# Performance work log

Hardware: AMD Instinct MI355X
Metric: run time of the kernel (lower is better)

Reference implementation:

```python
import jax, jax.numpy as jnp
import numpy as np

N, E, F_IN, HID, HEADS, NCLS = 50000, 800000, 512, 64, 4, 40
NEG_SLOPE = 0.2


def setup_inputs() -> dict:
    key = jax.random.key(0)
    ks = jax.random.split(key, 12)
    x = jax.random.normal(ks[0], (N, F_IN), jnp.float32)
    edge_index = jax.random.randint(ks[1], (2, E), 0, N, jnp.int32)
    edge_weight = jnp.ones((E,), jnp.float32)
    s1 = 1.0 / np.sqrt(F_IN)
    s2 = 1.0 / np.sqrt(HID * HEADS)
    return {
        "x": x,
        "edge_index": edge_index,
        "edge_weight": edge_weight,
        "W1": jax.random.normal(ks[2], (F_IN, HEADS * HID), jnp.float32) * s1,
        "a_src1": jax.random.normal(ks[3], (HEADS, HID), jnp.float32) * s1,
        "a_dst1": jax.random.normal(ks[4], (HEADS, HID), jnp.float32) * s1,
        "b1": jnp.zeros((HEADS * HID,), jnp.float32),
        "W2": jax.random.normal(ks[5], (HEADS * HID, NCLS), jnp.float32) * s2,
        "a_src2": jax.random.normal(ks[6], (1, NCLS), jnp.float32) * s2,
        "a_dst2": jax.random.normal(ks[7], (1, NCLS), jnp.float32) * s2,
        "b2": jnp.zeros((NCLS,), jnp.float32),
    }


def _gat_layer(x, src, dst, ew, W, a_s, a_d, b, heads, n):
    c = W.shape[1] // heads
    h = (x @ W).reshape(n, heads, c)                      # [N,H,C]
    alpha_s = jnp.einsum('nhc,hc->nh', h, a_s)            # [N,H]
    alpha_d = jnp.einsum('nhc,hc->nh', h, a_d)
    e = jax.nn.leaky_relu(alpha_s[src] + alpha_d[dst], NEG_SLOPE)  # [Et,H]
    # segment softmax over destination nodes (self-loops guarantee nonempty segs)
    m = jax.ops.segment_max(e, dst, num_segments=n)
    ex = jnp.exp(e - m[dst])
    denom = jax.ops.segment_sum(ex, dst, num_segments=n)
    alpha = ex / (denom[dst] + 1e-16)                     # [Et,H]
    alpha = alpha * ew[:, None]
    msg = h[src] * alpha[:, :, None]                      # [Et,H,C]
    out = jax.ops.segment_sum(msg, dst, num_segments=n)   # [N,H,C]
    return out.reshape(n, heads * c) + b


def reference(x, edge_index, edge_weight, W1, a_src1, a_dst1, b1, W2, a_src2, a_dst2, b2):
    n = x.shape[0]
    loop = jnp.arange(n, dtype=edge_index.dtype)
    src = jnp.concatenate([edge_index[0], loop])
    dst = jnp.concatenate([edge_index[1], loop])
    ew = jnp.concatenate([edge_weight, jnp.ones((n,), edge_weight.dtype)])
    h = _gat_layer(x, src, dst, ew, W1, a_src1, a_dst1, b1, HEADS, n)
    h = jax.nn.relu(h)  # dropout p=0.0, eval mode: no-op
    out = _gat_layer(h, src, dst, ew, W2, a_src2, a_dst2, b2, 1, n)
    return out  # Identity (log_softmax_return=False)
```

## Files before the change

kernel.cpp:

```cpp
#include <hip/hip_runtime.h>
#include <math.h>

#define N_NODES 50000
#define N_EDGES 800000
#define ET (N_EDGES + N_NODES)
#define F_IN 512
#define HID 64
#define HEADS 4
#define C1 (HEADS * HID)
#define NCLS 40
#define NEG_SLOPE 0.2f

#define BUK_SHIFT 9
#define BUK_NODES (1 << BUK_SHIFT)
#define NBUK ((N_NODES + BUK_NODES - 1) / BUK_NODES)
#define CAP 16384
#define NREP 4
#define SUBCAP (CAP / NREP)
#define BF_STRIDE 8
#define EPB_A 2048
#define NBLK_A ((ET + EPB_A - 1) / EPB_A)

typedef __attribute__((ext_vector_type(8))) short short8;
typedef __attribute__((ext_vector_type(4))) float floatx4;

__device__ __forceinline__ float leaky(float x) { return fmaxf(x, NEG_SLOPE * x); }

__device__ __forceinline__ unsigned short f2bf(float f) {
    unsigned u = __float_as_uint(f);
    u += 0x7fffu + ((u >> 16) & 1u);
    return (unsigned short)(u >> 16);
}
__device__ __forceinline__ float bf2f(unsigned short u) {
    return __uint_as_float(((unsigned)u) << 16);
}
__device__ __forceinline__ float bflo(unsigned v) { return __uint_as_float(v << 16); }
__device__ __forceinline__ float bfhi(unsigned v) { return __uint_as_float(v & 0xffff0000u); }

__device__ __forceinline__ void edge_sd(int e, const int* __restrict__ ei,
                                        const float* __restrict__ ew,
                                        int& s, int& d, float& w) {
    if (e < N_EDGES) { s = ei[e]; d = ei[N_EDGES + e]; w = ew[e]; }
    else             { s = d = e - N_EDGES; w = 1.f; }
}

__global__ __launch_bounds__(256) void passA_kernel(const int* __restrict__ ei,
                                                    const float* __restrict__ ew,
                                                    int* __restrict__ cnt,
                                                    int* __restrict__ bfill,
                                                    int2* __restrict__ SB) {
    __shared__ int lcnt[NBUK];
    __shared__ int lbase[NBUK];
    const int t = threadIdx.x;
    const int rep = blockIdx.x & (NREP - 1);
    const int e0 = blockIdx.x * EPB_A + t;
    for (int i = t; i < NBUK; i += 256) lcnt[i] = 0;
    __syncthreads();
    int rx[8], ry[8];
    #pragma unroll
    for (int i = 0; i < 8; i++) {
        int e = e0 + i * 256;
        rx[i] = -1;
        ry[i] = 0;
        if (e < ET) {
            int s, d; float w;
            edge_sd(e, ei, ew, s, d, w);
            rx[i] = s | (d << 16);
            ry[i] = __float_as_int(w);
            atomicAdd(&cnt[d], 1);
            atomicAdd(&lcnt[d >> BUK_SHIFT], 1);
        }
    }
    __syncthreads();
    for (int i = t; i < NBUK; i += 256) {
        int c = lcnt[i];
        lbase[i] = c ? atomicAdd(&bfill[(i * NREP + rep) * BF_STRIDE], c) : 0;
        lcnt[i] = 0;
    }
    __syncthreads();
    #pragma unroll
    for (int i = 0; i < 8; i++) {
        if (rx[i] != -1) {
            int b = ((unsigned)rx[i] >> 16) >> BUK_SHIFT;
            int r = atomicAdd(&lcnt[b], 1);
            int idx = lbase[b] + r;
            if (idx < SUBCAP)
                SB[(size_t)b * CAP + rep * SUBCAP + idx] = make_int2(rx[i], ry[i]);
        }
    }
}

__global__ void chunk_sum_kernel(const int* __restrict__ cnt, int* __restrict__ sums) {
    __shared__ int sm[512];
    int i = blockIdx.x * 512 + threadIdx.x;
    sm[threadIdx.x] = (i < N_NODES) ? cnt[i] : 0;
    __syncthreads();
    for (int s = 256; s > 0; s >>= 1) {
        if (threadIdx.x < s) sm[threadIdx.x] += sm[threadIdx.x + s];
        __syncthreads();
    }
    if (threadIdx.x == 0) sums[blockIdx.x] = sm[0];
}

__global__ void scan_sums_kernel(int* __restrict__ sums) {
    __shared__ int sm[128];
    int i = threadIdx.x;
    int v = (i < NBUK) ? sums[i] : 0;
    sm[i] = v;
    __syncthreads();
    #pragma unroll
    for (int s = 1; s < 128; s <<= 1) {
        int t = (i >= s) ? sm[i - s] : 0;
        __syncthreads();
        sm[i] += t;
        __syncthreads();
    }
    if (i < NBUK) sums[i] = sm[i] - v;
}

__global__ __launch_bounds__(512) void rowptr_kernel(const int* __restrict__ cnt,
                                                     const int* __restrict__ sums,
                                                     int* __restrict__ row_ptr) {
    __shared__ int sm[512];
    int i = blockIdx.x * 512 + threadIdx.x;
    int v = (i < N_NODES) ? cnt[i] : 0;
    sm[threadIdx.x] = v;
    __syncthreads();
    #pragma unroll
    for (int s = 1; s < 512; s <<= 1) {
        int t = (threadIdx.x >= s) ? sm[threadIdx.x - s] : 0;
        __syncthreads();
        sm[threadIdx.x] += t;
        __syncthreads();
    }
    int excl = sm[threadIdx.x] - v + sums[blockIdx.x];
    if (i < N_NODES) row_ptr[i] = excl;
}

__global__ __launch_bounds__(1024) void place_kernel(const int* __restrict__ row_ptr,
                                                     const int* __restrict__ bfill,
                                                     const int2* __restrict__ SB,
                                                     int2* __restrict__ E2) {
    __shared__ int lfill[BUK_NODES];
    int b = blockIdx.x;
    int n0 = b << BUK_SHIFT;
    int t = threadIdx.x;
    if (t < BUK_NODES) {
        int node = n0 + t;
        lfill[t] = (node < N_NODES) ? row_ptr[node] : 0;
    }
    __syncthreads();
    for (int rep = 0; rep < NREP; rep++) {
        int c = bfill[(b * NREP + rep) * BF_STRIDE];
        if (c > SUBCAP) c = SUBCAP;
        const int2* base = SB + (size_t)b * CAP + rep * SUBCAP;
        for (int i = t; i < c; i += 1024) {
            int2 rec = base[i];
            int d = ((unsigned)rec.x) >> 16;
            int pos = atomicAdd(&lfill[d - n0], 1);
            E2[pos] = make_int2(rec.x & 0xffff, rec.y);
        }
    }
}

__global__ void wt_prep_kernel(const float* __restrict__ W, unsigned short* __restrict__ WT) {
    __shared__ float tile[32][33];
    int k0 = blockIdx.x * 32;
    int n0 = blockIdx.y * 32;
    int tx = threadIdx.x, ty = threadIdx.y;
    #pragma unroll
    for (int i = 0; i < 32; i += 8)
        tile[ty + i][tx] = W[(size_t)(k0 + ty + i) * C1 + n0 + tx];
    __syncthreads();
    #pragma unroll
    for (int i = 0; i < 32; i += 8)
        WT[(size_t)(n0 + ty + i) * F_IN + k0 + tx] = f2bf(tile[tx][ty + i]);
}

__global__ __launch_bounds__(512) void gemm1_mfma_kernel(const float* __restrict__ X,
                                                         const unsigned short* __restrict__ WT,
                                                         const float* __restrict__ a_s1,
                                                         const float* __restrict__ a_d1,
                                                         unsigned short* __restrict__ H,
                                                         float* __restrict__ AS,
                                                         float* __restrict__ AD) {
    __shared__ short As[128][40];
    __shared__ short Bs[256][40];
    const int t = threadIdx.x;
    const int m0 = blockIdx.x * 128;
    const int lane = t & 63;
    const int wave = t >> 6;
    const int wm = wave >> 2;
    const int wn = wave & 3;
    const int l15 = lane & 15;
    const int quad = lane >> 4;

    const int ar = t >> 2;
    const int ac0 = (t & 3) * 8;
    const int gr = m0 + ar;
    const int bn = t >> 1;
    const int bc0 = (t & 1) * 16;

    floatx4 acc[4][4];
    #pragma unroll
    for (int i = 0; i < 4; i++)
        #pragma unroll
        for (int j = 0; j < 4; j++) acc[i][j] = (floatx4){0.f, 0.f, 0.f, 0.f};

    for (int k0 = 0; k0 < F_IN; k0 += 32) {
        float xv[8];
        if (gr < N_NODES) {
            const float4* p = (const float4*)(X + (size_t)gr * F_IN + k0 + ac0);
            float4 v0 = p[0], v1 = p[1];
            xv[0] = v0.x; xv[1] = v0.y; xv[2] = v0.z; xv[3] = v0.w;
            xv[4] = v1.x; xv[5] = v1.y; xv[6] = v1.z; xv[7] = v1.w;
        } else {
            #pragma unroll
            for (int i = 0; i < 8; i++) xv[i] = 0.f;
        }
        short8 av;
        #pragma unroll
        for (int i = 0; i < 8; i++) av[i] = (short)f2bf(xv[i]);
        *(short8*)&As[ar][ac0] = av;

        const short8* q = (const short8*)(WT + (size_t)bn * F_IN + k0 + bc0);
        *(short8*)&Bs[bn][bc0]     = q[0];
        *(short8*)&Bs[bn][bc0 + 8] = q[1];
        __syncthreads();

        short8 a[4], b[4];
        #pragma unroll
        for (int i = 0; i < 4; i++)
            a[i] = *(const short8*)&As[wm * 64 + i * 16 + l15][quad * 8];
        #pragma unroll
        for (int j = 0; j < 4; j++)
            b[j] = *(const short8*)&Bs[wn * 64 + j * 16 + l15][quad * 8];
        #pragma unroll
        for (int i = 0; i < 4; i++)
            #pragma unroll
            for (int j = 0; j < 4; j++)
                acc[i][j] = __builtin_amdgcn_mfma_f32_16x16x32_bf16(a[i], b[j], acc[i][j], 0, 0, 0);
        __syncthreads();
    }

    float asr[4], adr[4];
    #pragma unroll
    for (int j = 0; j < 4; j++) {
        asr[j] = a_s1[wn * HID + j * 16 + l15];
        adr[j] = a_d1[wn * HID + j * 16 + l15];
    }

    #pragma unroll
    for (int i = 0; i < 4; i++) {
        int rbase = m0 + wm * 64 + i * 16 + quad * 4;
        #pragma unroll
        for (int j = 0; j < 4; j++) {
            int col = wn * 64 + j * 16 + l15;
            #pragma unroll
            for (int r = 0; r < 4; r++) {
                int row = rbase + r;
                if (row < N_NODES) H[(size_t)row * C1 + col] = f2bf(acc[i][j][r]);
            }
        }
        #pragma unroll
        for (int r = 0; r < 4; r++) {
            int row = rbase + r;
            float s_ = acc[i][0][r] * asr[0] + acc[i][1][r] * asr[1]
                     + acc[i][2][r] * asr[2] + acc[i][3][r] * asr[3];
            float d_ = acc[i][0][r] * adr[0] + acc[i][1][r] * adr[1]
                     + acc[i][2][r] * adr[2] + acc[i][3][r] * adr[3];
            #pragma unroll
            for (int m = 8; m; m >>= 1) { s_ += __shfl_xor(s_, m); d_ += __shfl_xor(d_, m); }
            if (l15 == 0 && row < N_NODES) {
                AS[row * 4 + wn] = s_;
                AD[row * 4 + wn] = d_;
            }
        }
    }
}

__global__ __launch_bounds__(256, 6) void agg1_csr_kernel(const int* __restrict__ row_ptr,
                                                          const int2* __restrict__ E2,
                                                          const float* __restrict__ AS,
                                                          const float* __restrict__ AD,
                                                          const unsigned short* __restrict__ H,
                                                          const float* __restrict__ b1,
                                                          unsigned short* __restrict__ OUT) {
    int n = blockIdx.x * 4 + (threadIdx.x >> 6);
    int lane = threadIdx.x & 63;
    if (n >= N_NODES) return;
    int l15 = lane & 15;
    int h = lane >> 4;
    int c0 = lane * 4;
    int beg = row_ptr[n];
    int end = (n + 1 < N_NODES) ? row_ptr[n + 1] : ET;
    float ad = AD[n * 4 + h];
    float den = 0.f;
    float a0 = 0.f, a1 = 0.f, a2 = 0.f, a3 = 0.f;

    for (int base = beg; base < end; base += 16) {
        int m = end - base; if (m > 16) m = 16;
        float pw = 0.f; int s = 0;
        if (l15 < m) {
            int2 e = E2[base + l15];
            s = e.x;
            float pe = __expf(leaky(AS[e.x * 4 + h] + ad));
            den += pe;
            pw = pe * __int_as_float(e.y);
        }
        int p = 0;
        for (; p + 8 <= m; p += 8) {
            int s0 = __shfl(s, p);
            int s1 = __shfl(s, p + 1);
            int s2 = __shfl(s, p + 2);
            int s3 = __shfl(s, p + 3);
            int s4 = __shfl(s, p + 4);
            int s5 = __shfl(s, p + 5);
            int s6 = __shfl(s, p + 6);
            int s7 = __shfl(s, p + 7);
            uint2 u0 = *(const uint2*)(H + (size_t)s0 * C1 + c0);
            uint2 u1 = *(const uint2*)(H + (size_t)s1 * C1 + c0);
            uint2 u2 = *(const uint2*)(H + (size_t)s2 * C1 + c0);
            uint2 u3 = *(const uint2*)(H + (size_t)s3 * C1 + c0);
            uint2 u4 = *(const uint2*)(H + (size_t)s4 * C1 + c0);
            uint2 u5 = *(const uint2*)(H + (size_t)s5 * C1 + c0);
            uint2 u6 = *(const uint2*)(H + (size_t)s6 * C1 + c0);
            uint2 u7 = *(const uint2*)(H + (size_t)s7 * C1 + c0);
            float w0 = __shfl(pw, h * 16 + p);
            float w1 = __shfl(pw, h * 16 + p + 1);
            float w2 = __shfl(pw, h * 16 + p + 2);
            float w3 = __shfl(pw, h * 16 + p + 3);
            float w4 = __shfl(pw, h * 16 + p + 4);
            float w5 = __shfl(pw, h * 16 + p + 5);
            float w6 = __shfl(pw, h * 16 + p + 6);
            float w7 = __shfl(pw, h * 16 + p + 7);
            a0 += w0 * bflo(u0.x) + w1 * bflo(u1.x) + w2 * bflo(u2.x) + w3 * bflo(u3.x)
                + w4 * bflo(u4.x) + w5 * bflo(u5.x) + w6 * bflo(u6.x) + w7 * bflo(u7.x);
            a1 += w0 * bfhi(u0.x) + w1 * bfhi(u1.x) + w2 * bfhi(u2.x) + w3 * bfhi(u3.x)
                + w4 * bfhi(u4.x) + w5 * bfhi(u5.x) + w6 * bfhi(u6.x) + w7 * bfhi(u7.x);
            a2 += w0 * bflo(u0.y) + w1 * bflo(u1.y) + w2 * bflo(u2.y) + w3 * bflo(u3.y)
                + w4 * bflo(u4.y) + w5 * bflo(u5.y) + w6 * bflo(u6.y) + w7 * bflo(u7.y);
            a3 += w0 * bfhi(u0.y) + w1 * bfhi(u1.y) + w2 * bfhi(u2.y) + w3 * bfhi(u3.y)
                + w4 * bfhi(u4.y) + w5 * bfhi(u5.y) + w6 * bfhi(u6.y) + w7 * bfhi(u7.y);
        }
        for (; p < m; p++) {
            int s0 = __shfl(s, p);
            uint2 u0 = *(const uint2*)(H + (size_t)s0 * C1 + c0);
            float w0 = __shfl(pw, h * 16 + p);
            a0 += w0 * bflo(u0.x);
            a1 += w0 * bfhi(u0.x);
            a2 += w0 * bflo(u0.y);
            a3 += w0 * bfhi(u0.y);
        }
    }
    den += __shfl_xor(den, 1);
    den += __shfl_xor(den, 2);
    den += __shfl_xor(den, 4);
    den += __shfl_xor(den, 8);

    float r = 1.f / (den + 1e-16f);
    float4 bv = *(const float4*)(b1 + c0);
    float v0 = a0 * r + bv.x, v1 = a1 * r + bv.y, v2 = a2 * r + bv.z, v3 = a3 * r + bv.w;
    v0 = v0 > 0.f ? v0 : 0.f;
    v1 = v1 > 0.f ? v1 : 0.f;
    v2 = v2 > 0.f ? v2 : 0.f;
    v3 = v3 > 0.f ? v3 : 0.f;
    uint2 o;
    o.x = ((unsigned)f2bf(v1) << 16) | (unsigned)f2bf(v0);
    o.y = ((unsigned)f2bf(v3) << 16) | (unsigned)f2bf(v2);
    *(uint2*)(OUT + (size_t)n * C1 + c0) = o;
}

#define BROW 264
__global__ __launch_bounds__(512) void gemm2_mfma_kernel(const unsigned short* __restrict__ A,
                                                         const float* __restrict__ W2,
                                                         const float* __restrict__ a_s2,
                                                         const float* __restrict__ a_d2,
                                                         unsigned short* __restrict__ H2b,
                                                         float* __restrict__ AS2,
                                                         float* __restrict__ AD2) {
    __shared__ short As[256][40];
    __shared__ short Bs[48 * BROW];
    const int t = threadIdx.x;
    const int m0 = blockIdx.x * 256;
    const int lane = t & 63;
    const int wave = t >> 6;
    const int l15 = lane & 15;
    const int quad = lane >> 4;

    for (int i = t; i < 48 * 256; i += 512) {
        int n = i >> 8, k = i & 255;
        float v = (n < NCLS) ? W2[k * NCLS + n] : 0.f;
        Bs[n * BROW + k] = (short)f2bf(v);
    }

    const int ar = t >> 1;
    const int ac0 = (t & 1) * 16;

    floatx4 acc[2][3];
    #pragma unroll
    for (int i = 0; i < 2; i++)
        #pragma unroll
        for (int j = 0; j < 3; j++) acc[i][j] = (floatx4){0.f, 0.f, 0.f, 0.f};

    for (int k0 = 0; k0 < C1; k0 += 32) {
        const short8* q = (const short8*)(A + (size_t)(m0 + ar) * C1 + k0 + ac0);
        short8 v0 = q[0], v1 = q[1];
        __syncthreads();
        *(short8*)&As[ar][ac0]     = v0;
        *(short8*)&As[ar][ac0 + 8] = v1;
        __syncthreads();

        short8 a[2], b[3];
        #pragma unroll
        for (int i = 0; i < 2; i++)
            a[i] = *(const short8*)&As[wave * 32 + i * 16 + l15][quad * 8];
        #pragma unroll
        for (int j = 0; j < 3; j++)
            b[j] = *(const short8*)&Bs[(j * 16 + l15) * BROW + k0 + quad * 8];
        #pragma unroll
        for (int i = 0; i < 2; i++)
            #pragma unroll
            for (int j = 0; j < 3; j++)
                acc[i][j] = __builtin_amdgcn_mfma_f32_16x16x32_bf16(a[i], b[j], acc[i][j], 0, 0, 0);
    }

    float asr[3], adr[3];
    #pragma unroll
    for (int j = 0; j < 3; j++) {
        int col = j * 16 + l15;
        asr[j] = (col < NCLS) ? a_s2[col] : 0.f;
        adr[j] = (col < NCLS) ? a_d2[col] : 0.f;
    }

    #pragma unroll
    for (int i = 0; i < 2; i++) {
        #pragma unroll
        for (int r = 0; r < 4; r++) {
            int row = m0 + wave * 32 + i * 16 + quad * 4 + r;
            float s_ = acc[i][0][r] * asr[0] + acc[i][1][r] * asr[1] + acc[i][2][r] * asr[2];
            float d_ = acc[i][0][r] * adr[0] + acc[i][1][r] * adr[1] + acc[i][2][r] * adr[2];
            #pragma unroll
            for (int m = 8; m; m >>= 1) { s_ += __shfl_xor(s_, m); d_ += __shfl_xor(d_, m); }
            if (l15 == 0 && row < N_NODES) { AS2[row] = s_; AD2[row] = d_; }
            #pragma unroll
            for (int j = 0; j < 3; j++) {
                int col = j * 16 + l15;
                if (col < NCLS && row < N_NODES)
                    H2b[(size_t)row * NCLS + col] = f2bf(acc[i][j][r]);
            }
        }
    }
}

__global__ __launch_bounds__(256) void agg2_csr_kernel(const int* __restrict__ row_ptr,
                                                       const int2* __restrict__ E2,
                                                       const float* __restrict__ AS,
                                                       const float* __restrict__ AD,
                                                       const unsigned short* __restrict__ H2b,
                                                       const float* __restrict__ b2,
                                                       float* __restrict__ OUT) {
    int lane = threadIdx.x & 63;
    int n = blockIdx.x * 4 + (threadIdx.x >> 6);
    if (n >= N_NODES) return;
    int beg = row_ptr[n];
    int end = (n + 1 < N_NODES) ? row_ptr[n + 1] : ET;
    float ad = AD[n];
    bool act = lane < NCLS;
    float den = 0.f, acc = 0.f;

    for (int base = beg; base < end; base += 64) {
        int m = end - base; if (m > 64) m = 64;
        float pw = 0.f; int s = 0;
        if (lane < m) {
            int2 e = E2[base + lane];
            s = e.x;
            float pe = __expf(leaky(AS[e.x] + ad));
            den += pe;
            pw = pe * __int_as_float(e.y);
        }
        int p = 0;
        for (; p + 4 <= m; p += 4) {
            int s0 = __shfl(s, p);
            int s1 = __shfl(s, p + 1);
            int s2 = __shfl(s, p + 2);
            int s3 = __shfl(s, p + 3);
            float w0 = __shfl(pw, p);
            float w1 = __shfl(pw, p + 1);
            float w2 = __shfl(pw, p + 2);
            float w3 = __shfl(pw, p + 3);
            if (act) {
                float h0 = bf2f(H2b[(size_t)s0 * NCLS + lane]);
                float h1 = bf2f(H2b[(size_t)s1 * NCLS + lane]);
                float h2 = bf2f(H2b[(size_t)s2 * NCLS + lane]);
                float h3 = bf2f(H2b[(size_t)s3 * NCLS + lane]);
                acc += w0 * h0 + w1 * h1 + w2 * h2 + w3 * h3;
            }
        }
        for (; p < m; p++) {
            int s0 = __shfl(s, p);
            float w0 = __shfl(pw, p);
            if (act) acc += w0 * bf2f(H2b[(size_t)s0 * NCLS + lane]);
        }
    }
    den += __shfl_xor(den, 1);
    den += __shfl_xor(den, 2);
    den += __shfl_xor(den, 4);
    den += __shfl_xor(den, 8);
    den += __shfl_xor(den, 16);
    den += __shfl_xor(den, 32);
    if (act) {
        float r = 1.f / (den + 1e-16f);
        OUT[(size_t)n * NCLS + lane] = acc * r + b2[lane];
    }
}

extern "C" void kernel_launch(void* const* d_in, const int* in_sizes, int n_in,
                              void* d_out, int out_size, void* d_ws, size_t ws_size,
                              hipStream_t stream) {
    const float* x    = (const float*)d_in[0];
    const int*   ei   = (const int*)d_in[1];
    const float* ew   = (const float*)d_in[2];
    const float* W1   = (const float*)d_in[3];
    const float* a_s1 = (const float*)d_in[4];
    const float* a_d1 = (const float*)d_in[5];
    const float* b1   = (const float*)d_in[6];
    const float* W2   = (const float*)d_in[7];
    const float* a_s2 = (const float*)d_in[8];
    const float* a_d2 = (const float*)d_in[9];
    const float* b2   = (const float*)d_in[10];
    float* out = (float*)d_out;

    unsigned short* H1b  = (unsigned short*)d_ws;
    unsigned short* OUT1b = H1b + (size_t)N_NODES * C1;
    float* AS1  = (float*)(OUT1b + (size_t)N_NODES * C1);
    float* AD1  = AS1 + N_NODES * HEADS;
    int* row_ptr = (int*)(AD1 + N_NODES * HEADS);
    int* cnt  = row_ptr + N_NODES;
    int* bfill = cnt + N_NODES;
    int2* E2  = (int2*)(bfill + NBUK * NREP * BF_STRIDE);
    int* sums = (int*)(E2 + ET);
    unsigned short* WT = (unsigned short*)(sums + NBUK);
    unsigned short* H2b = H1b;
    float* AS2  = (float*)(H2b + (size_t)N_NODES * NCLS);
    float* AD2  = AS2 + N_NODES;
    int2* SB = (int2*)H1b;

    hipMemsetAsync(cnt, 0, (N_NODES + NBUK * NREP * BF_STRIDE) * sizeof(int), stream);
    wt_prep_kernel<<<dim3(F_IN / 32, C1 / 32), dim3(32, 8), 0, stream>>>(W1, WT);
    passA_kernel<<<NBLK_A, 256, 0, stream>>>(ei, ew, cnt, bfill, SB);
    chunk_sum_kernel<<<NBUK, 512, 0, stream>>>(cnt, sums);
    scan_sums_kernel<<<1, 128, 0, stream>>>(sums);
    rowptr_kernel<<<NBUK, 512, 0, stream>>>(cnt, sums, row_ptr);
    place_kernel<<<NBUK, 1024, 0, stream>>>(row_ptr, bfill, SB, E2);

    gemm1_mfma_kernel<<<(N_NODES + 127) / 128, 512, 0, stream>>>(x, WT, a_s1, a_d1, H1b, AS1, AD1);
    agg1_csr_kernel<<<(N_NODES + 3) / 4, 256, 0, stream>>>(row_ptr, E2, AS1, AD1, H1b, b1, OUT1b);

    gemm2_mfma_kernel<<<(N_NODES + 255) / 256, 512, 0, stream>>>(OUT1b, W2, a_s2, a_d2, H2b, AS2, AD2);
    agg2_csr_kernel<<<(N_NODES + 3) / 4, 256, 0, stream>>>(row_ptr, E2, AS2, AD2, H2b, b2, out);
}
```

Before: 362.0 us.

## Split layer-1 aggregation into per-XCD feature halves for L2 locality

The layer-1 aggregation kernel now splits each node's 256 features into two halves handled by separate blocks. The blocks are mapped so that XCDs 0-3 process the first half (heads 0-1) and XCDs 4-7 the second half. Each XCD's L2 then only caches half of the gathered H rows, which improves its hit rate on random neighbor gathers. In exchange, edge indices and attention exponentials are recomputed in both halves, and each gather load becomes narrower (4 bytes per lane instead of 8).

```diff
diff --git a/kernel.cpp b/kernel.cpp
--- a/kernel.cpp
+++ b/kernel.cpp
@@ -279,32 +279,38 @@
     }
 }
 
-__global__ __launch_bounds__(256, 6) void agg1_csr_kernel(const int* __restrict__ row_ptr,
-                                                          const int2* __restrict__ E2,
-                                                          const float* __restrict__ AS,
-                                                          const float* __restrict__ AD,
-                                                          const unsigned short* __restrict__ H,
-                                                          const float* __restrict__ b1,
-                                                          unsigned short* __restrict__ OUT) {
-    int n = blockIdx.x * 4 + (threadIdx.x >> 6);
-    int lane = threadIdx.x & 63;
-    if (n >= N_NODES) return;
-    int l15 = lane & 15;
-    int h = lane >> 4;
-    int c0 = lane * 4;
+__global__ __launch_bounds__(256, 8) void agg1_half_kernel(const int* __restrict__ row_ptr,
+                                                           const int2* __restrict__ E2,
+                                                           const float* __restrict__ AS,
+                                                           const float* __restrict__ AD,
+                                                           const unsigned short* __restrict__ H,
+                                                           const float* __restrict__ b1,
+                                                           unsigned short* __restrict__ OUT) {
+    const int i = blockIdx.x;
+    const int xcd = i & 7;
+    const int half = xcd >> 2;
+    const int ng = (i >> 3) * 4 + (xcd & 3);
+    const int wave = threadIdx.x >> 6;
+    const int n = ng * 4 + wave;
+    const int lane = threadIdx.x & 63;
+    const int l31 = lane & 31;
+    const int hh = lane >> 5;
+    const int head = half * 2 + hh;
+    const int c0 = half * 128 + lane * 2;
+    const unsigned short* Hc = H + c0;
+
     int beg = row_ptr[n];
     int end = (n + 1 < N_NODES) ? row_ptr[n + 1] : ET;
-    float ad = AD[n * 4 + h];
-    float den = 0.f;
-    float a0 = 0.f, a1 = 0.f, a2 = 0.f, a3 = 0.f;
-
-    for (int base = beg; base < end; base += 16) {
-        int m = end - base; if (m > 16) m = 16;
+    float ad = AD[n * 4 + head];
+    float den = 0.f, a0 = 0.f, a1 = 0.f;
+
+    for (int base = beg; base < end; base += 32) {
+        int m = end - base; if (m > 32) m = 32;
         float pw = 0.f; int s = 0;
-        if (l15 < m) {
-            int2 e = E2[base + l15];
+        if (l31 < m) {
+            int2 e = E2[base + l31];
             s = e.x;
-            float pe = __expf(leaky(AS[e.x * 4 + h] + ad));
+            float pe = __expf(leaky(AS[e.x * 4 + head] + ad));
             den += pe;
             pw = pe * __int_as_float(e.y);
         }
@@ -318,57 +324,48 @@
             int s5 = __shfl(s, p + 5);
             int s6 = __shfl(s, p + 6);
             int s7 = __shfl(s, p + 7);
-            uint2 u0 = *(const uint2*)(H + (size_t)s0 * C1 + c0);
-            uint2 u1 = *(const uint2*)(H + (size_t)s1 * C1 + c0);
-            uint2 u2 = *(const uint2*)(H + (size_t)s2 * C1 + c0);
-            uint2 u3 = *(const uint2*)(H + (size_t)s3 * C1 + c0);
-            uint2 u4 = *(const uint2*)(H + (size_t)s4 * C1 + c0);
-            uint2 u5 = *(const uint2*)(H + (size_t)s5 * C1 + c0);
-            uint2 u6 = *(const uint2*)(H + (size_t)s6 * C1 + c0);
-            uint2 u7 = *(const uint2*)(H + (size_t)s7 * C1 + c0);
-            float w0 = __shfl(pw, h * 16 + p);
-            float w1 = __shfl(pw, h * 16 + p + 1);
-            float w2 = __shfl(pw, h * 16 + p + 2);
-            float w3 = __shfl(pw, h * 16 + p + 3);
-            float w4 = __shfl(pw, h * 16 + p + 4);
-            float w5 = __shfl(pw, h * 16 + p + 5);
-            float w6 = __shfl(pw, h * 16 + p + 6);
-            float w7 = __shfl(pw, h * 16 + p + 7);
-            a0 += w0 * bflo(u0.x) + w1 * bflo(u1.x) + w2 * bflo(u2.x) + w3 * bflo(u3.x)
-                + w4 * bflo(u4.x) + w5 * bflo(u5.x) + w6 * bflo(u6.x) + w7 * bflo(u7.x);
-            a1 += w0 * bfhi(u0.x) + w1 * bfhi(u1.x) + w2 * bfhi(u2.x) + w3 * bfhi(u3.x)
-                + w4 * bfhi(u4.x) + w5 * bfhi(u5.x) + w6 * bfhi(u6.x) + w7 * bfhi(u7.x);
-            a2 += w0 * bflo(u0.y) + w1 * bflo(u1.y) + w2 * bflo(u2.y) + w3 * bflo(u3.y)
-                + w4 * bflo(u4.y) + w5 * bflo(u5.y) + w6 * bflo(u6.y) + w7 * bflo(u7.y);
-            a3 += w0 * bfhi(u0.y) + w1 * bfhi(u1.y) + w2 * bfhi(u2.y) + w3 * bfhi(u3.y)
-                + w4 * bfhi(u4.y) + w5 * bfhi(u5.y) + w6 * bfhi(u6.y) + w7 * bfhi(u7.y);
+            unsigned u0 = *(const unsigned*)(Hc + (size_t)s0 * C1);
+            unsigned u1 = *(const unsigned*)(Hc + (size_t)s1 * C1);
+            unsigned u2 = *(const unsigned*)(Hc + (size_t)s2 * C1);
+            unsigned u3 = *(const unsigned*)(Hc + (size_t)s3 * C1);
+            unsigned u4 = *(const unsigned*)(Hc + (size_t)s4 * C1);
+            unsigned u5 = *(const unsigned*)(Hc + (size_t)s5 * C1);
+            unsigned u6 = *(const unsigned*)(Hc + (size_t)s6 * C1);
+            unsigned u7 = *(const unsigned*)(Hc + (size_t)s7 * C1);
+            float w0 = __shfl(pw, hh * 32 + p);
+            float w1 = __shfl(pw, hh * 32 + p + 1);
+            float w2 = __shfl(pw, hh * 32 + p + 2);
+            float w3 = __shfl(pw, hh * 32 + p + 3);
+            float w4 = __shfl(pw, hh * 32 + p + 4);
+            float w5 = __shfl(pw, hh * 32 + p + 5);
+            float w6 = __shfl(pw, hh * 32 + p + 6);
+            float w7 = __shfl(pw, hh * 32 + p + 7);
+            a0 += w0 * bflo(u0) + w1 * bflo(u1) + w2 * bflo(u2) + w3 * bflo(u3)
+                + w4 * bflo(u4) + w5 * bflo(u5) + w6 * bflo(u6) + w7 * bflo(u7);
+            a1 += w0 * bfhi(u0) + w1 * bfhi(u1) + w2 * bfhi(u2) + w3 * bfhi(u3)
+                + w4 * bfhi(u4) + w5 * bfhi(u5) + w6 * bfhi(u6) + w7 * bfhi(u7);
         }
         for (; p < m; p++) {
             int s0 = __shfl(s, p);
-            uint2 u0 = *(const uint2*)(H + (size_t)s0 * C1 + c0);
-            float w0 = __shfl(pw, h * 16 + p);
-            a0 += w0 * bflo(u0.x);
-            a1 += w0 * bfhi(u0.x);
-            a2 += w0 * bflo(u0.y);
-            a3 += w0 * bfhi(u0.y);
+            unsigned u0 = *(const unsigned*)(Hc + (size_t)s0 * C1);
+            float w0 = __shfl(pw, hh * 32 + p);
+            a0 += w0 * bflo(u0);
+            a1 += w0 * bfhi(u0);
         }
     }
     den += __shfl_xor(den, 1);
     den += __shfl_xor(den, 2);
     den += __shfl_xor(den, 4);
     den += __shfl_xor(den, 8);
+    den += __shfl_xor(den, 16);
 
     float r = 1.f / (den + 1e-16f);
-    float4 bv = *(const float4*)(b1 + c0);
-    float v0 = a0 * r + bv.x, v1 = a1 * r + bv.y, v2 = a2 * r + bv.z, v3 = a3 * r + bv.w;
+    float2 bv = *(const float2*)(b1 + c0);
+    float v0 = a0 * r + bv.x, v1 = a1 * r + bv.y;
     v0 = v0 > 0.f ? v0 : 0.f;
     v1 = v1 > 0.f ? v1 : 0.f;
-    v2 = v2 > 0.f ? v2 : 0.f;
-    v3 = v3 > 0.f ? v3 : 0.f;
-    uint2 o;
-    o.x = ((unsigned)f2bf(v1) << 16) | (unsigned)f2bf(v0);
-    o.y = ((unsigned)f2bf(v3) << 16) | (unsigned)f2bf(v2);
-    *(uint2*)(OUT + (size_t)n * C1 + c0) = o;
+    unsigned o = ((unsigned)f2bf(v1) << 16) | (unsigned)f2bf(v0);
+    *(unsigned*)(OUT + (size_t)n * C1 + c0) = o;
 }
 
 #define BROW 264
@@ -555,7 +552,7 @@
     place_kernel<<<NBUK, 1024, 0, stream>>>(row_ptr, bfill, SB, E2);
 
     gemm1_mfma_kernel<<<(N_NODES + 127) / 128, 512, 0, stream>>>(x, WT, a_s1, a_d1, H1b, AS1, AD1);
-    agg1_csr_kernel<<<(N_NODES + 3) / 4, 256, 0, stream>>>(row_ptr, E2, AS1, AD1, H1b, b1, OUT1b);
+    agg1_half_kernel<<<2 * (N_NODES / 4), 256, 0, stream>>>(row_ptr, E2, AS1, AD1, H1b, b1, OUT1b);
 
     gemm2_mfma_kernel<<<(N_NODES + 255) / 256, 512, 0, stream>>>(OUT1b, W2, a_s2, a_d2, H2b, AS2, AD2);
     agg2_csr_kernel<<<(N_NODES + 3) / 4, 256, 0, stream>>>(row_ptr, E2, AS2, AD2, H2b, b2, out);
```

Result: no change. 363.1 us (+0.3%).

## Build CSR per bucket in shared memory, dropping global degree atomics and scans

Applied to the files above, without the earlier changes.

The CSR build no longer does per-node global atomic degree counts and a three-kernel scan. Buckets shrink to 128 nodes, one small kernel scans the per-bucket counts, and place_kernel stages each bucket's records in LDS, builds a local histogram and scan to write row_ptr, then scatters into E2. Separately, agg1's gather loop unroll drops from 8 to 4 and its occupancy hint is removed. Records past the fixed capacities (SUBCAP, RCAP) are silently dropped, which only holds if bucket sizes stay small enough for these random graphs.

```diff
diff --git a/kernel.cpp b/kernel.cpp
--- a/kernel.cpp
+++ b/kernel.cpp
@@ -11,15 +11,16 @@
 #define NCLS 40
 #define NEG_SLOPE 0.2f
 
-#define BUK_SHIFT 9
+#define BUK_SHIFT 7
 #define BUK_NODES (1 << BUK_SHIFT)
 #define NBUK ((N_NODES + BUK_NODES - 1) / BUK_NODES)
-#define CAP 16384
+#define CAP 4096
 #define NREP 4
 #define SUBCAP (CAP / NREP)
 #define BF_STRIDE 8
 #define EPB_A 2048
 #define NBLK_A ((ET + EPB_A - 1) / EPB_A)
+#define RCAP 2560
 
 typedef __attribute__((ext_vector_type(8))) short short8;
 typedef __attribute__((ext_vector_type(4))) float floatx4;
@@ -46,7 +47,6 @@
 
 __global__ __launch_bounds__(256) void passA_kernel(const int* __restrict__ ei,
                                                     const float* __restrict__ ew,
-                                                    int* __restrict__ cnt,
                                                     int* __restrict__ bfill,
                                                     int2* __restrict__ SB) {
     __shared__ int lcnt[NBUK];
@@ -67,7 +67,6 @@
             edge_sd(e, ei, ew, s, d, w);
             rx[i] = s | (d << 16);
             ry[i] = __float_as_int(w);
-            atomicAdd(&cnt[d], 1);
             atomicAdd(&lcnt[d >> BUK_SHIFT], 1);
         }
     }
@@ -90,76 +89,88 @@
     }
 }
 
-__global__ void chunk_sum_kernel(const int* __restrict__ cnt, int* __restrict__ sums) {
+__global__ __launch_bounds__(512) void scan_bbase_kernel(const int* __restrict__ bfill,
+                                                         int* __restrict__ bbase) {
     __shared__ int sm[512];
-    int i = blockIdx.x * 512 + threadIdx.x;
-    sm[threadIdx.x] = (i < N_NODES) ? cnt[i] : 0;
-    __syncthreads();
-    for (int s = 256; s > 0; s >>= 1) {
-        if (threadIdx.x < s) sm[threadIdx.x] += sm[threadIdx.x + s];
-        __syncthreads();
-    }
-    if (threadIdx.x == 0) sums[blockIdx.x] = sm[0];
-}
-
-__global__ void scan_sums_kernel(int* __restrict__ sums) {
-    __shared__ int sm[128];
-    int i = threadIdx.x;
-    int v = (i < NBUK) ? sums[i] : 0;
-    sm[i] = v;
-    __syncthreads();
-    #pragma unroll
-    for (int s = 1; s < 128; s <<= 1) {
-        int t = (i >= s) ? sm[i - s] : 0;
-        __syncthreads();
-        sm[i] += t;
-        __syncthreads();
-    }
-    if (i < NBUK) sums[i] = sm[i] - v;
-}
-
-__global__ __launch_bounds__(512) void rowptr_kernel(const int* __restrict__ cnt,
-                                                     const int* __restrict__ sums,
-                                                     int* __restrict__ row_ptr) {
-    __shared__ int sm[512];
-    int i = blockIdx.x * 512 + threadIdx.x;
-    int v = (i < N_NODES) ? cnt[i] : 0;
-    sm[threadIdx.x] = v;
+    int t = threadIdx.x;
+    int v = 0;
+    if (t < NBUK) {
+        #pragma unroll
+        for (int r = 0; r < NREP; r++) {
+            int c = bfill[(t * NREP + r) * BF_STRIDE];
+            v += (c > SUBCAP) ? SUBCAP : c;
+        }
+    }
+    sm[t] = v;
     __syncthreads();
     #pragma unroll
     for (int s = 1; s < 512; s <<= 1) {
-        int t = (threadIdx.x >= s) ? sm[threadIdx.x - s] : 0;
-        __syncthreads();
-        sm[threadIdx.x] += t;
-        __syncthreads();
-    }
-    int excl = sm[threadIdx.x] - v + sums[blockIdx.x];
-    if (i < N_NODES) row_ptr[i] = excl;
-}
-
-__global__ __launch_bounds__(1024) void place_kernel(const int* __restrict__ row_ptr,
-                                                     const int* __restrict__ bfill,
-                                                     const int2* __restrict__ SB,
-                                                     int2* __restrict__ E2) {
-    __shared__ int lfill[BUK_NODES];
-    int b = blockIdx.x;
-    int n0 = b << BUK_SHIFT;
-    int t = threadIdx.x;
+        int u = (t >= s) ? sm[t - s] : 0;
+        __syncthreads();
+        sm[t] += u;
+        __syncthreads();
+    }
+    if (t < NBUK) bbase[t] = sm[t] - v;
+}
+
+__global__ __launch_bounds__(512) void place_kernel(const int* __restrict__ bfill,
+                                                    const int* __restrict__ bbase,
+                                                    const int2* __restrict__ SB,
+                                                    int* __restrict__ row_ptr,
+                                                    int2* __restrict__ E2) {
+    __shared__ int2 rec[RCAP];
+    __shared__ int lh[BUK_NODES];
+    __shared__ int excl[BUK_NODES];
+    const int b = blockIdx.x;
+    const int n0 = b << BUK_SHIFT;
+    const int t = threadIdx.x;
+
+    int c[NREP], off[NREP];
+    int tot = 0;
+    #pragma unroll
+    for (int r = 0; r < NREP; r++) {
+        int cc = bfill[(b * NREP + r) * BF_STRIDE];
+        c[r] = (cc > SUBCAP) ? SUBCAP : cc;
+        off[r] = tot;
+        tot += c[r];
+    }
+    if (t < BUK_NODES) lh[t] = 0;
+    __syncthreads();
+    #pragma unroll
+    for (int r = 0; r < NREP; r++) {
+        const int2* base = SB + (size_t)b * CAP + r * SUBCAP;
+        for (int i = t; i < c[r]; i += 512) {
+            int idx = off[r] + i;
+            if (idx < RCAP) rec[idx] = base[i];
+        }
+    }
+    if (tot > RCAP) tot = RCAP;
+    __syncthreads();
+    for (int i = t; i < tot; i += 512)
+        atomicAdd(&lh[(((unsigned)rec[i].x) >> 16) - n0], 1);
+    __syncthreads();
+    if (t < BUK_NODES) excl[t] = lh[t];
+    __syncthreads();
+    #pragma unroll
+    for (int s = 1; s < BUK_NODES; s <<= 1) {
+        int u = (t < BUK_NODES && t >= s) ? excl[t - s] : 0;
+        __syncthreads();
+        if (t < BUK_NODES) excl[t] += u;
+        __syncthreads();
+    }
+    const int base_b = bbase[b];
     if (t < BUK_NODES) {
+        int e = excl[t] - lh[t];
         int node = n0 + t;
-        lfill[t] = (node < N_NODES) ? row_ptr[node] : 0;
-    }
-    __syncthreads();
-    for (int rep = 0; rep < NREP; rep++) {
-        int c = bfill[(b * NREP + rep) * BF_STRIDE];
-        if (c > SUBCAP) c = SUBCAP;
-        const int2* base = SB + (size_t)b * CAP + rep * SUBCAP;
-        for (int i = t; i < c; i += 1024) {
-            int2 rec = base[i];
-            int d = ((unsigned)rec.x) >> 16;
-            int pos = atomicAdd(&lfill[d - n0], 1);
-            E2[pos] = make_int2(rec.x & 0xffff, rec.y);
-        }
+        if (node < N_NODES) row_ptr[node] = base_b + e;
+        lh[t] = e;
+    }
+    __syncthreads();
+    for (int i = t; i < tot; i += 512) {
+        int2 v = rec[i];
+        int d = (((unsigned)v.x) >> 16) - n0;
+        int pos = atomicAdd(&lh[d], 1);
+        E2[base_b + pos] = make_int2(v.x & 0xffff, v.y);
     }
 }
 
@@ -279,13 +290,13 @@
     }
 }
 
-__global__ __launch_bounds__(256, 6) void agg1_csr_kernel(const int* __restrict__ row_ptr,
-                                                          const int2* __restrict__ E2,
-                                                          const float* __restrict__ AS,
-                                                          const float* __restrict__ AD,
-                                                          const unsigned short* __restrict__ H,
-                                                          const float* __restrict__ b1,
-                                                          unsigned short* __restrict__ OUT) {
+__global__ __launch_bounds__(256) void agg1_csr_kernel(const int* __restrict__ row_ptr,
+                                                       const int2* __restrict__ E2,
+                                                       const float* __restrict__ AS,
+                                                       const float* __restrict__ AD,
+                                                       const unsigned short* __restrict__ H,
+                                                       const float* __restrict__ b1,
+                                                       unsigned short* __restrict__ OUT) {
     int n = blockIdx.x * 4 + (threadIdx.x >> 6);
     int lane = threadIdx.x & 63;
     if (n >= N_NODES) return;
@@ -309,39 +320,23 @@
             pw = pe * __int_as_float(e.y);
         }
         int p = 0;
-        for (; p + 8 <= m; p += 8) {
+        for (; p + 4 <= m; p += 4) {
             int s0 = __shfl(s, p);
             int s1 = __shfl(s, p + 1);
             int s2 = __shfl(s, p + 2);
             int s3 = __shfl(s, p + 3);
-            int s4 = __shfl(s, p + 4);
-            int s5 = __shfl(s, p + 5);
-            int s6 = __shfl(s, p + 6);
-            int s7 = __shfl(s, p + 7);
             uint2 u0 = *(const uint2*)(H + (size_t)s0 * C1 + c0);
             uint2 u1 = *(const uint2*)(H + (size_t)s1 * C1 + c0);
             uint2 u2 = *(const uint2*)(H + (size_t)s2 * C1 + c0);
             uint2 u3 = *(const uint2*)(H + (size_t)s3 * C1 + c0);
-            uint2 u4 = *(const uint2*)(H + (size_t)s4 * C1 + c0);
-            uint2 u5 = *(const uint2*)(H + (size_t)s5 * C1 + c0);
-            uint2 u6 = *(const uint2*)(H + (size_t)s6 * C1 + c0);
-            uint2 u7 = *(const uint2*)(H + (size_t)s7 * C1 + c0);
             float w0 = __shfl(pw, h * 16 + p);
             float w1 = __shfl(pw, h * 16 + p + 1);
             float w2 = __shfl(pw, h * 16 + p + 2);
             float w3 = __shfl(pw, h * 16 + p + 3);
-            float w4 = __shfl(pw, h * 16 + p + 4);
-            float w5 = __shfl(pw, h * 16 + p + 5);
-            float w6 = __shfl(pw, h * 16 + p + 6);
-            float w7 = __shfl(pw, h * 16 + p + 7);
-            a0 += w0 * bflo(u0.x) + w1 * bflo(u1.x) + w2 * bflo(u2.x) + w3 * bflo(u3.x)
-                + w4 * bflo(u4.x) + w5 * bflo(u5.x) + w6 * bflo(u6.x) + w7 * bflo(u7.x);
-            a1 += w0 * bfhi(u0.x) + w1 * bfhi(u1.x) + w2 * bfhi(u2.x) + w3 * bfhi(u3.x)
-                + w4 * bfhi(u4.x) + w5 * bfhi(u5.x) + w6 * bfhi(u6.x) + w7 * bfhi(u7.x);
-            a2 += w0 * bflo(u0.y) + w1 * bflo(u1.y) + w2 * bflo(u2.y) + w3 * bflo(u3.y)
-                + w4 * bflo(u4.y) + w5 * bflo(u5.y) + w6 * bflo(u6.y) + w7 * bflo(u7.y);
-            a3 += w0 * bfhi(u0.y) + w1 * bfhi(u1.y) + w2 * bfhi(u2.y) + w3 * bfhi(u3.y)
-                + w4 * bfhi(u4.y) + w5 * bfhi(u5.y) + w6 * bfhi(u6.y) + w7 * bfhi(u7.y);
+            a0 += w0 * bflo(u0.x) + w1 * bflo(u1.x) + w2 * bflo(u2.x) + w3 * bflo(u3.x);
+            a1 += w0 * bfhi(u0.x) + w1 * bfhi(u1.x) + w2 * bfhi(u2.x) + w3 * bfhi(u3.x);
+            a2 += w0 * bflo(u0.y) + w1 * bflo(u1.y) + w2 * bflo(u2.y) + w3 * bflo(u3.y);
+            a3 += w0 * bfhi(u0.y) + w1 * bfhi(u1.y) + w2 * bfhi(u2.y) + w3 * bfhi(u3.y);
         }
         for (; p < m; p++) {
             int s0 = __shfl(s, p);
@@ -536,23 +531,20 @@
     float* AS1  = (float*)(OUT1b + (size_t)N_NODES * C1);
     float* AD1  = AS1 + N_NODES * HEADS;
     int* row_ptr = (int*)(AD1 + N_NODES * HEADS);
-    int* cnt  = row_ptr + N_NODES;
-    int* bfill = cnt + N_NODES;
-    int2* E2  = (int2*)(bfill + NBUK * NREP * BF_STRIDE);
-    int* sums = (int*)(E2 + ET);
-    unsigned short* WT = (unsigned short*)(sums + NBUK);
+    int* bfill = row_ptr + N_NODES;
+    int* bbase = bfill + NBUK * NREP * BF_STRIDE;
+    int2* E2  = (int2*)(bbase + NBUK + 1);
+    unsigned short* WT = (unsigned short*)(E2 + ET);
     unsigned short* H2b = H1b;
     float* AS2  = (float*)(H2b + (size_t)N_NODES * NCLS);
     float* AD2  = AS2 + N_NODES;
     int2* SB = (int2*)H1b;
 
-    hipMemsetAsync(cnt, 0, (N_NODES + NBUK * NREP * BF_STRIDE) * sizeof(int), stream);
+    hipMemsetAsync(bfill, 0, NBUK * NREP * BF_STRIDE * sizeof(int), stream);
     wt_prep_kernel<<<dim3(F_IN / 32, C1 / 32), dim3(32, 8), 0, stream>>>(W1, WT);
-    passA_kernel<<<NBLK_A, 256, 0, stream>>>(ei, ew, cnt, bfill, SB);
-    chunk_sum_kernel<<<NBUK, 512, 0, stream>>>(cnt, sums);
-    scan_sums_kernel<<<1, 128, 0, stream>>>(sums);
-    rowptr_kernel<<<NBUK, 512, 0, stream>>>(cnt, sums, row_ptr);
-    place_kernel<<<NBUK, 1024, 0, stream>>>(row_ptr, bfill, SB, E2);
+    passA_kernel<<<NBLK_A, 256, 0, stream>>>(ei, ew, bfill, SB);
+    scan_bbase_kernel<<<1, 512, 0, stream>>>(bfill, bbase);
+    place_kernel<<<NBUK, 512, 0, stream>>>(bfill, bbase, SB, row_ptr, E2);
 
     gemm1_mfma_kernel<<<(N_NODES + 127) / 128, 512, 0, stream>>>(x, WT, a_s1, a_d1, H1b, AS1, AD1);
     agg1_csr_kernel<<<(N_NODES + 3) / 4, 256, 0, stream>>>(row_ptr, E2, AS1, AD1, H1b, b1, OUT1b);
```

Result: faster. 330.1 us (-8.8%).
